# Kernel tuning notes

Measured on AMD Instinct MI355X. Metric: run time of the kernel, lower is better.

## Reference

```python
import jax, jax.numpy as jnp
import numpy as np
import math

N_HEADS = 16
N_POINTS = 4
EPS = 1e-6


def layer_norm(x, g, b):
    m = x.mean(-1, keepdims=True)
    v = ((x - m) ** 2).mean(-1, keepdims=True)
    return (x - m) / jnp.sqrt(v + EPS) * g + b


def ref_points(H, W, dtype):
    # matches CrossSelfAtt.get_reference_points for one square level -> (1, H*W, 1, 2) in (x, y)
    ys = (jnp.arange(H, dtype=dtype) + 0.5) / H
    xs = (jnp.arange(W, dtype=dtype) + 0.5) / W
    gy, gx = jnp.meshgrid(ys, xs, indexing='ij')
    return jnp.stack([gx.reshape(-1), gy.reshape(-1)], -1)[None, :, None, :]


def bilinear(v, H, W, loc):
    # v: (B, H*W, nH, Dh); loc: (B, Lq, nH, P, 2) normalized [0,1]; zero padding, align_corners=False
    B, _, nH, Dh = v.shape
    Lq, P = loc.shape[1], loc.shape[3]
    x = loc[..., 0] * W - 0.5
    y = loc[..., 1] * H - 0.5
    x0 = jnp.floor(x)
    y0 = jnp.floor(y)
    wx1 = x - x0
    wy1 = y - y0
    x0i = x0.astype(jnp.int32)
    y0i = y0.astype(jnp.int32)
    vt = v.transpose(0, 2, 1, 3)  # (B, nH, HW, Dh)

    def corner(xi, yi, w):
        valid = (xi >= 0) & (xi < W) & (yi >= 0) & (yi < H)
        idx = jnp.clip(yi, 0, H - 1) * W + jnp.clip(xi, 0, W - 1)  # (B, Lq, nH, P)
        idx_t = idx.transpose(0, 2, 1, 3).reshape(B, nH, Lq * P)
        g = jnp.take_along_axis(vt, idx_t[..., None], axis=2).reshape(B, nH, Lq, P, Dh)
        return g.transpose(0, 2, 1, 3, 4) * (w * valid)[..., None]

    return (corner(x0i, y0i, (1 - wx1) * (1 - wy1))
            + corner(x0i + 1, y0i, wx1 * (1 - wy1))
            + corner(x0i, y0i + 1, (1 - wx1) * wy1)
            + corner(x0i + 1, y0i + 1, wx1 * wy1))


def msda(query, value_in, shapes, ref, Wv, bv, Woff, boff, Wa, ba, Wo, bo):
    # standard Deformable-DETR MSDeformAttn forward
    B, Lq, D = query.shape
    nH, P, L = N_HEADS, N_POINTS, len(shapes)
    Dh = D // nH
    value = (value_in @ Wv + bv).reshape(B, -1, nH, Dh)
    off = (query @ Woff + boff).reshape(B, Lq, nH, L, P, 2)
    aw = jax.nn.softmax((query @ Wa + ba).reshape(B, Lq, nH, L * P), -1).reshape(B, Lq, nH, L, P)
    norm = jnp.asarray([[w_, h_] for (h_, w_) in shapes], dtype=query.dtype)  # (L, 2) = (W, H)
    loc = ref[:, :, None, :, None, :] + off / norm[None, None, None, :, None, :]
    out = jnp.zeros((B, Lq, nH, Dh), query.dtype)
    start = 0
    for l, (H_, W_) in enumerate(shapes):
        samp = bilinear(value[:, start:start + H_ * W_], H_, W_, loc[:, :, :, l])
        out = out + (samp * aw[:, :, :, l, :, None]).sum(3)
        start += H_ * W_
    return out.reshape(B, Lq, D) @ Wo + bo


def setup_inputs() -> dict:
    key = jax.random.key(0)
    B, Lq, Lf, D = 2, 4096, 4096, 768
    nH, P, L = N_HEADS, N_POINTS, 1
    ks = jax.random.split(key, 20)
    w = lambda k, s: jax.random.normal(k, s, jnp.float32) * 0.02
    return {
        'query': jax.random.normal(ks[0], (B, Lq, D), jnp.float32),
        'feat': jax.random.normal(ks[1], (B, Lf, D), jnp.float32),
        'spatial_shapes': jnp.array([[64, 64]], jnp.int32),
        'level_start_index': jnp.array([0], jnp.int32),
        'qn_W': w(ks[2], (D, D)), 'qn_b': jnp.zeros((D,)), 'qn_g': jnp.ones((D,)), 'qn_beta': jnp.zeros((D,)),
        'fn_W': w(ks[3], (D, D)), 'fn_b': jnp.zeros((D,)), 'fn_g': jnp.ones((D,)), 'fn_beta': jnp.zeros((D,)),
        'nm_g': jnp.ones((D,)), 'nm_beta': jnp.zeros((D,)),
        'gamma1': jax.random.normal(ks[4], (D,), jnp.float32) * 0.1,
        'c_Wv': w(ks[5], (D, D)), 'c_bv': jnp.zeros((D,)),
        'c_Woff': w(ks[6], (D, nH * L * P * 2)),
        'c_boff': jax.random.uniform(ks[7], (nH * L * P * 2,), jnp.float32, -3.0, 3.0),
        'c_Wa': w(ks[8], (D, nH * L * P)), 'c_ba': jnp.zeros((nH * L * P,)),
        'c_Wo': w(ks[9], (D, D)), 'c_bo': jnp.zeros((D,)),
        's_Wv': w(ks[10], (D, D)), 's_bv': jnp.zeros((D,)),
        's_Woff': w(ks[11], (D, nH * L * P * 2)),
        's_boff': jax.random.uniform(ks[12], (nH * L * P * 2,), jnp.float32, -3.0, 3.0),
        's_Wa': w(ks[13], (D, nH * L * P)), 's_ba': jnp.zeros((nH * L * P,)),
        's_Wo': w(ks[14], (D, D)), 's_bo': jnp.zeros((D,)),
    }


def reference(query, feat, spatial_shapes, level_start_index, qn_W, qn_b, qn_g, qn_beta, fn_W, fn_b, fn_g, fn_beta, nm_g, nm_beta, gamma1, c_Wv, c_bv, c_Woff, c_boff, c_Wa, c_ba, c_Wo, c_bo, s_Wv, s_bv, s_Woff, s_boff, s_Wa, s_ba, s_Wo, s_bo):
    shapes = [(int(h), int(w_)) for h, w_ in np.asarray(spatial_shapes)]
    qe = int(math.sqrt(query.shape[1]))
    ref = ref_points(qe, qe, query.dtype)  # (1, Lq, 1, 2)
    qn = layer_norm(query @ qn_W + qn_b, qn_g, qn_beta)
    fn = layer_norm(feat @ fn_W + fn_b, fn_g, fn_beta)
    attn = msda(qn, fn, shapes, ref, c_Wv, c_bv, c_Woff, c_boff, c_Wa, c_ba, c_Wo, c_bo)
    attn1 = layer_norm(attn, nm_g, nm_beta)
    attn2 = msda(attn1, attn1, [(qe, qe)], ref, s_Wv, s_bv, s_Woff, s_boff, s_Wa, s_ba, s_Wo, s_bo)
    # note: source uses gamma1 for BOTH terms (gamma2 is unused)
    return attn * gamma1 + attn2 * gamma1
```

## Files before the change

kernel.cpp:

```cpp
#include <hip/hip_runtime.h>
#include <hip/hip_bf16.h>
#include <math.h>

#define D_MODEL 768
#define NH 16
#define DH 48
#define NP 4
#define LQ 4096
#define BB 2
#define MTOT (BB * LQ)

typedef __attribute__((ext_vector_type(8))) _Float16 half8_t;
typedef __attribute__((ext_vector_type(4))) float floatx4;

__device__ __forceinline__ void load_lds16(const void* g, void* l) {
    __builtin_amdgcn_global_load_lds((const __attribute__((address_space(1))) void*)g,
                                     (__attribute__((address_space(3))) void*)l, 16, 0, 0);
}

template <int MODE>
__device__ __forceinline__ void gemm_body(
    const _Float16* __restrict__ A, const _Float16* __restrict__ Wt,
    const float* __restrict__ bias, float* __restrict__ C, int ldc,
    int tm, int tn,
    const float* __restrict__ attn, const float* __restrict__ gamma)
{
    constexpr int K = 768;
    constexpr int NT = K / 32;
    __shared__ _Float16 As[2][128 * 32];
    __shared__ _Float16 Bs[2][128 * 32];

    const int bm = tm * 128, bn = tn * 128;
    const int t = threadIdx.x;
    const int lane = t & 63;
    const int w = t >> 6;
    const int wm = (w >> 1) * 64, wn = (w & 1) * 64;

    floatx4 acc[4][4] = {};

    const int r0 = t >> 2;
    const int c8 = (t & 3) * 8;
    const size_t arow0 = (size_t)(bm + r0) * K + c8;
    const size_t arow1 = (size_t)(bm + 64 + r0) * K + c8;
    const size_t brow0 = (size_t)(bn + r0) * K + c8;
    const size_t brow1 = (size_t)(bn + 64 + r0) * K + c8;

    const int lrow = lane & 15;
    const int lk = (lane >> 4) * 8;

    load_lds16(A + arow0, &As[0][w * 512]);
    load_lds16(A + arow1, &As[0][2048 + w * 512]);
    load_lds16(Wt + brow0, &Bs[0][w * 512]);
    load_lds16(Wt + brow1, &Bs[0][2048 + w * 512]);
    __syncthreads();

    for (int ti = 0; ti < NT; ++ti) {
        const int cur = ti & 1;
        if (ti + 1 < NT) {
            const int kn = (ti + 1) * 32;
            const int nxt = cur ^ 1;
            load_lds16(A + arow0 + kn, &As[nxt][w * 512]);
            load_lds16(A + arow1 + kn, &As[nxt][2048 + w * 512]);
            load_lds16(Wt + brow0 + kn, &Bs[nxt][w * 512]);
            load_lds16(Wt + brow1 + kn, &Bs[nxt][2048 + w * 512]);
        }

        const _Float16* Ac = As[cur];
        const _Float16* Bc = Bs[cur];
        half8_t af[4], bf[4];
#pragma unroll
        for (int i = 0; i < 4; ++i) {
            af[i] = *(const half8_t*)&Ac[(wm + i * 16 + lrow) * 32 + lk];
            bf[i] = *(const half8_t*)&Bc[(wn + i * 16 + lrow) * 32 + lk];
        }
#pragma unroll
        for (int i = 0; i < 4; ++i)
#pragma unroll
            for (int j = 0; j < 4; ++j)
                acc[i][j] = __builtin_amdgcn_mfma_f32_16x16x32_f16(af[i], bf[j], acc[i][j], 0, 0, 0);

        if (ti + 1 < NT) __syncthreads();
    }

    const int rquad = (lane >> 4) * 4;
#pragma unroll
    for (int i = 0; i < 4; ++i) {
#pragma unroll
        for (int j = 0; j < 4; ++j) {
            const int col = bn + wn + j * 16 + lrow;
            const float bcol = bias[col];
#pragma unroll
            for (int r = 0; r < 4; ++r) {
                const size_t row = (size_t)(bm + wm + i * 16 + rquad + r);
                float v = acc[i][j][r] + bcol;
                if (MODE == 1) v = (attn[row * ldc + col] + v) * gamma[col];
                C[row * (size_t)ldc + col] = v;
            }
        }
    }
}

template <int MODE>
__global__ __launch_bounds__(256) void gemm_mfma(
    const _Float16* __restrict__ A, const _Float16* __restrict__ Wt,
    const float* __restrict__ bias, float* __restrict__ C,
    const float* __restrict__ attn, const float* __restrict__ gamma)
{
    const int bid = blockIdx.x;
    const int swz = (bid & 7) * 48 + (bid >> 3);
    gemm_body<MODE>(A, Wt, bias, C, 768, swz & 63, swz >> 6, attn, gamma);
}

__global__ __launch_bounds__(256) void dual_gemm(
    const _Float16* __restrict__ A0, const _Float16* __restrict__ W0,
    const float* __restrict__ b0, float* __restrict__ C0, int ldc0, int cnt0,
    const _Float16* __restrict__ A1, const _Float16* __restrict__ W1,
    const float* __restrict__ b1, float* __restrict__ C1, int ldc1, int cnt1)
{
    int bid = blockIdx.x;
    const _Float16 *A, *Wt; const float* bias; float* C; int ldc, cnt;
    if (bid < cnt0) { A = A0; Wt = W0; bias = b0; C = C0; ldc = ldc0; cnt = cnt0; }
    else { bid -= cnt0; A = A1; Wt = W1; bias = b1; C = C1; ldc = ldc1; cnt = cnt1; }
    const int q = cnt >> 3;
    const int swz = (bid & 7) * q + (bid >> 3);
    gemm_body<0>(A, Wt, bias, C, ldc, swz & 63, swz >> 6, nullptr, nullptr);
}

__device__ __forceinline__ void ln_wave_body(
    const float* __restrict__ X, _Float16* __restrict__ A,
    const float* __restrict__ g, const float* __restrict__ beta, int row)
{
    const int lane = threadIdx.x & 63;
    const float* x = X + (size_t)row * D_MODEL;
    float v[12];
    float s = 0.f, s2 = 0.f;
#pragma unroll
    for (int j = 0; j < 12; ++j) {
        v[j] = x[lane + 64 * j];
        s += v[j];
        s2 += v[j] * v[j];
    }
#pragma unroll
    for (int m = 1; m < 64; m <<= 1) {
        s += __shfl_xor(s, m);
        s2 += __shfl_xor(s2, m);
    }
    const float mean = s * (1.f / 768.f);
    const float var = s2 * (1.f / 768.f) - mean * mean;
    const float rstd = rsqrtf(var + 1e-6f);
    _Float16* arow = A + (size_t)row * D_MODEL;
#pragma unroll
    for (int j = 0; j < 12; ++j) {
        const int cc = lane + 64 * j;
        arow[cc] = (_Float16)((v[j] - mean) * rstd * g[cc] + beta[cc]);
    }
}

__global__ __launch_bounds__(256) void ln2_wave(
    const float* __restrict__ X0, _Float16* __restrict__ A0,
    const float* __restrict__ g0, const float* __restrict__ b0,
    const float* __restrict__ X1, _Float16* __restrict__ A1,
    const float* __restrict__ g1, const float* __restrict__ b1)
{
    const int r = blockIdx.x * 4 + (threadIdx.x >> 6);
    if (r < MTOT) ln_wave_body(X0, A0, g0, b0, r);
    else          ln_wave_body(X1, A1, g1, b1, r - MTOT);
}

__global__ __launch_bounds__(256) void ln_wave(
    const float* __restrict__ X, _Float16* __restrict__ A,
    const float* __restrict__ g, const float* __restrict__ beta)
{
    const int r = blockIdx.x * 4 + (threadIdx.x >> 6);
    ln_wave_body(X, A, g, beta, r);
}

__global__ __launch_bounds__(256) void convert_act2(
    const float* __restrict__ X0, _Float16* __restrict__ D0,
    const float* __restrict__ X1, _Float16* __restrict__ D1)
{
    const int i = blockIdx.x * 256 + threadIdx.x;
    const int sel = i / (MTOT * 192);
    const int r = i - sel * (MTOT * 192);
    const float* X = sel ? X1 : X0;
    _Float16* D = sel ? D1 : D0;
    const int c4 = r * 4;
    const float4 v = *(const float4*)(X + (size_t)c4);
    _Float16 o[4] = {(_Float16)v.x, (_Float16)v.y, (_Float16)v.z, (_Float16)v.w};
    *(uint2*)(D + (size_t)c4) = *(uint2*)o;
}

__global__ __launch_bounds__(256) void convert_w6(
    const float* __restrict__ w0, const float* __restrict__ w1,
    const float* __restrict__ w2, const float* __restrict__ w3,
    const float* __restrict__ w4, const float* __restrict__ w5,
    _Float16* __restrict__ Wall)
{
    const int wi = blockIdx.y;
    const float* W = (wi == 0) ? w0 : (wi == 1) ? w1 : (wi == 2) ? w2
                   : (wi == 3) ? w3 : (wi == 4) ? w4 : w5;
    _Float16* Wt = Wall + (size_t)wi * 768 * 768;

    __shared__ float tile[32][33];
    const int tk0 = (blockIdx.x / 24) * 32;
    const int tn0 = (blockIdx.x % 24) * 32;
    const int t = threadIdx.x;
#pragma unroll
    for (int r = 0; r < 4; ++r) {
        const int row = r * 8 + (t >> 5);
        const int col = t & 31;
        tile[row][col] = W[(size_t)(tk0 + row) * 768 + tn0 + col];
    }
    __syncthreads();
    const int n = t >> 3;
    const int kq = (t & 7) * 4;
    _Float16* dst = Wt + (size_t)(tn0 + n) * 768 + tk0 + kq;
#pragma unroll
    for (int u = 0; u < 4; ++u) dst[u] = (_Float16)tile[kq + u][n];
}

__global__ __launch_bounds__(256) void convert_offa(
    const float* __restrict__ Woff_c, const float* __restrict__ Wa_c,
    const float* __restrict__ boff_c, const float* __restrict__ ba_c,
    const float* __restrict__ Woff_s, const float* __restrict__ Wa_s,
    const float* __restrict__ boff_s, const float* __restrict__ ba_s,
    _Float16* __restrict__ Wc, _Float16* __restrict__ Ws,
    float* __restrict__ bias_c, float* __restrict__ bias_s)
{
    const int i = blockIdx.x * 256 + threadIdx.x;
    if (i >= 2 * 256 * 192) return;
    const int pair = i / (256 * 192);
    const int r = i - pair * (256 * 192);
    const int n = r / 192;
    const int k0 = (r - n * 192) * 4;
    const float* Woff = pair ? Woff_s : Woff_c;
    const float* Wa = pair ? Wa_s : Wa_c;
    _Float16* dst = pair ? Ws : Wc;
    _Float16* row = dst + (size_t)n * 768;
#pragma unroll
    for (int u = 0; u < 4; ++u) {
        const int k = k0 + u;
        float v = (n < 128) ? Woff[(size_t)k * 128 + n]
                : (n < 192) ? Wa[(size_t)k * 64 + (n - 128)] : 0.f;
        row[k] = (_Float16)v;
    }
    if (k0 == 0) {
        const float* boff = pair ? boff_s : boff_c;
        const float* ba = pair ? ba_s : ba_c;
        float* bias = pair ? bias_s : bias_c;
        bias[n] = (n < 128) ? boff[n] : (n < 192) ? ba[n - 128] : 0.f;
    }
}

__global__ __launch_bounds__(256) void offaw_post(
    const float* __restrict__ offc,
    float* __restrict__ loc, float* __restrict__ aw)
{
    const int i = blockIdx.x * 256 + threadIdx.x;
    if (i >= MTOT * NH) return;
    const int h = i & (NH - 1);
    const int bq = i >> 4;
    const int q = bq & (LQ - 1);

    const float* orow = offc + (size_t)bq * 256 + h * 8;
    const float* arow = offc + (size_t)bq * 256 + 128 + h * 4;

    float a0 = arow[0], a1 = arow[1], a2 = arow[2], a3 = arow[3];
    float mx = fmaxf(fmaxf(a0, a1), fmaxf(a2, a3));
    float e0 = expf(a0 - mx), e1 = expf(a1 - mx), e2 = expf(a2 - mx), e3 = expf(a3 - mx);
    float r = 1.f / (e0 + e1 + e2 + e3);

    const float refx = ((q & 63) + 0.5f) * (1.f / 64.f);
    const float refy = ((q >> 6) + 0.5f) * (1.f / 64.f);
#pragma unroll
    for (int p = 0; p < 4; ++p) {
        loc[(size_t)i * 8 + p * 2 + 0] = refx + orow[p * 2 + 0] * (1.f / 64.f);
        loc[(size_t)i * 8 + p * 2 + 1] = refy + orow[p * 2 + 1] * (1.f / 64.f);
    }
    aw[(size_t)i * 4 + 0] = e0 * r;
    aw[(size_t)i * 4 + 1] = e1 * r;
    aw[(size_t)i * 4 + 2] = e2 * r;
    aw[(size_t)i * 4 + 3] = e3 * r;
}

__global__ __launch_bounds__(256) void sample_f4(
    const float* __restrict__ value, const float* __restrict__ loc,
    const float* __restrict__ aw, _Float16* __restrict__ A)
{
    const int bid = blockIdx.x;
    const int swz = (bid & 7) * 768 + (bid >> 3);
    const int idx = swz * 256 + threadIdx.x;
    const int bqh = idx / 12;
    const int c = idx - bqh * 12;
    const int d0 = c * 4;
    const int h = bqh & (NH - 1);
    const int bq = bqh >> 4;
    const int b = bq >> 12;

    const float4 l01 = *(const float4*)(loc + (size_t)bqh * 8);
    const float4 l23 = *(const float4*)(loc + (size_t)bqh * 8 + 4);
    const float4 w4 = *(const float4*)(aw + (size_t)bqh * 4);
    const float lx[4] = {l01.x, l01.z, l23.x, l23.z};
    const float ly[4] = {l01.y, l01.w, l23.y, l23.w};
    const float wp4[4] = {w4.x, w4.y, w4.z, w4.w};

    const float* vbase = value + (size_t)b * LQ * D_MODEL + h * DH + d0;

    float4 acc = {0.f, 0.f, 0.f, 0.f};
#pragma unroll
    for (int p = 0; p < 4; ++p) {
        const float x = lx[p] * 64.f - 0.5f;
        const float y = ly[p] * 64.f - 0.5f;
        const float xf = floorf(x), yf = floorf(y);
        const float wx1 = x - xf, wy1 = y - yf;
        const float wx0 = 1.f - wx1, wy0 = 1.f - wy1;
        const int x0 = (int)xf, y0 = (int)yf;
        const int x1 = x0 + 1, y1 = y0 + 1;
        const float wp = wp4[p];
        const bool vx0 = (x0 >= 0) && (x0 < 64);
        const bool vx1 = (x1 >= 0) && (x1 < 64);
        const bool vy0 = (y0 >= 0) && (y0 < 64);
        const bool vy1 = (y1 >= 0) && (y1 < 64);
        const float cw[4] = {wp * wx0 * wy0, wp * wx1 * wy0, wp * wx0 * wy1, wp * wx1 * wy1};
        const bool cv[4] = {vx0 && vy0, vx1 && vy0, vx0 && vy1, vx1 && vy1};
        const int cxy[4][2] = {{x0, y0}, {x1, y0}, {x0, y1}, {x1, y1}};
#pragma unroll
        for (int k = 0; k < 4; ++k) {
            if (cv[k]) {
                const float4 g = *(const float4*)(vbase + (size_t)(cxy[k][1] * 64 + cxy[k][0]) * D_MODEL);
                acc.x += cw[k] * g.x; acc.y += cw[k] * g.y;
                acc.z += cw[k] * g.z; acc.w += cw[k] * g.w;
            }
        }
    }

    _Float16* arow = A + (size_t)bq * D_MODEL + h * DH + d0;
    _Float16 o[4] = {(_Float16)acc.x, (_Float16)acc.y, (_Float16)acc.z, (_Float16)acc.w};
    *(uint2*)arow = *(uint2*)o;
}

extern "C" void kernel_launch(void* const* d_in, const int* in_sizes, int n_in,
                              void* d_out, int out_size, void* d_ws, size_t ws_size,
                              hipStream_t stream)
{
    const float* query   = (const float*)d_in[0];
    const float* feat    = (const float*)d_in[1];
    const float* qn_W    = (const float*)d_in[4];
    const float* qn_b    = (const float*)d_in[5];
    const float* qn_g    = (const float*)d_in[6];
    const float* qn_beta = (const float*)d_in[7];
    const float* fn_W    = (const float*)d_in[8];
    const float* fn_b    = (const float*)d_in[9];
    const float* fn_g    = (const float*)d_in[10];
    const float* fn_beta = (const float*)d_in[11];
    const float* nm_g    = (const float*)d_in[12];
    const float* nm_beta = (const float*)d_in[13];
    const float* gamma1  = (const float*)d_in[14];
    const float* c_Wv    = (const float*)d_in[15];
    const float* c_bv    = (const float*)d_in[16];
    const float* c_Woff  = (const float*)d_in[17];
    const float* c_boff  = (const float*)d_in[18];
    const float* c_Wa    = (const float*)d_in[19];
    const float* c_ba    = (const float*)d_in[20];
    const float* c_Wo    = (const float*)d_in[21];
    const float* c_bo    = (const float*)d_in[22];
    const float* s_Wv    = (const float*)d_in[23];
    const float* s_bv    = (const float*)d_in[24];
    const float* s_Woff  = (const float*)d_in[25];
    const float* s_boff  = (const float*)d_in[26];
    const float* s_Wa    = (const float*)d_in[27];
    const float* s_ba    = (const float*)d_in[28];
    const float* s_Wo    = (const float*)d_in[29];
    const float* s_bo    = (const float*)d_in[30];

    float* ws = (float*)d_ws;
    const size_t SZ = (size_t)MTOT * D_MODEL;
    float* buf0 = ws;
    float* buf1 = ws + SZ;
    float* buf2 = ws + 2 * SZ;
    float* buf3 = ws + 3 * SZ;
    _Float16* slotA = (_Float16*)(ws + 4 * SZ);
    _Float16* slotB = (_Float16*)(ws + 4 * SZ + SZ / 2);
    float* loc    = ws + 5 * SZ;
    float* aws    = loc + (size_t)MTOT * 128;
    float* bias_c = aws + (size_t)MTOT * 64;
    float* bias_s = bias_c + 256;
    _Float16* W6 = (_Float16*)(bias_s + 256);
    _Float16* W_qn  = W6 + (size_t)0 * 768 * 768;
    _Float16* W_fn  = W6 + (size_t)1 * 768 * 768;
    _Float16* W_cWv = W6 + (size_t)2 * 768 * 768;
    _Float16* W_cWo = W6 + (size_t)3 * 768 * 768;
    _Float16* W_sWv = W6 + (size_t)4 * 768 * 768;
    _Float16* W_sWo = W6 + (size_t)5 * 768 * 768;
    _Float16* Woffa_c = W6 + (size_t)6 * 768 * 768;
    _Float16* Woffa_s = Woffa_c + (size_t)256 * 768;

    float* out = (float*)d_out;
    const dim3 blk(256);

    convert_w6<<<dim3(576, 6), blk, 0, stream>>>(qn_W, fn_W, c_Wv, c_Wo, s_Wv, s_Wo, W6);
    convert_offa<<<384, blk, 0, stream>>>(c_Woff, c_Wa, c_boff, c_ba,
                                          s_Woff, s_Wa, s_boff, s_ba,
                                          Woffa_c, Woffa_s, bias_c, bias_s);
    convert_act2<<<12288, blk, 0, stream>>>(query, slotA, feat, slotB);

    dual_gemm<<<768, blk, 0, stream>>>(slotA, W_qn, qn_b, buf0, 768, 384,
                                       slotB, W_fn, fn_b, buf1, 768, 384);
    ln2_wave<<<2 * MTOT / 4, blk, 0, stream>>>(buf0, slotA, qn_g, qn_beta,
                                               buf1, slotB, fn_g, fn_beta);
    dual_gemm<<<512, blk, 0, stream>>>(slotB, W_cWv, c_bv, buf2, 768, 384,
                                       slotA, Woffa_c, bias_c, buf0, 256, 128);
    offaw_post<<<(MTOT * NH + 255) / 256, blk, 0, stream>>>(buf0, loc, aws);
    sample_f4<<<MTOT * NH * 12 / 256, blk, 0, stream>>>(buf2, loc, aws, slotB);
    gemm_mfma<0><<<384, blk, 0, stream>>>(slotB, W_cWo, c_bo, buf3, nullptr, nullptr);

    ln_wave<<<MTOT / 4, blk, 0, stream>>>(buf3, slotA, nm_g, nm_beta);
    dual_gemm<<<512, blk, 0, stream>>>(slotA, W_sWv, s_bv, buf2, 768, 384,
                                       slotA, Woffa_s, bias_s, buf0, 256, 128);
    offaw_post<<<(MTOT * NH + 255) / 256, blk, 0, stream>>>(buf0, loc, aws);
    sample_f4<<<MTOT * NH * 12 / 256, blk, 0, stream>>>(buf2, loc, aws, slotB);
    gemm_mfma<1><<<384, blk, 0, stream>>>(slotB, W_sWo, s_bo, out, buf3, gamma1);
}
```

Measured before the change: 382.4 us.

## Store value projection in fp16, fuse offset post-processing into sampler, merge convert kernels

The value projection GEMM now writes fp16 output, and the bilinear sampler gathers half8 vectors instead of float4, which halves the gather traffic. The softmax and location computation from offaw_post moves into the sampler through shared memory, so the loc and aw round-trip through global memory and one launch per attention stage go away. The three conversion kernels become a single launch. The costs are fp16 rounding of the value tensor and 192-thread blocks in the sampler, where 32 threads do the preprocessing while the rest wait at a barrier.

```diff
diff --git a/kernel.cpp b/kernel.cpp
--- a/kernel.cpp
+++ b/kernel.cpp
@@ -21,7 +21,7 @@
 template <int MODE>
 __device__ __forceinline__ void gemm_body(
     const _Float16* __restrict__ A, const _Float16* __restrict__ Wt,
-    const float* __restrict__ bias, float* __restrict__ C, int ldc,
+    const float* __restrict__ bias, void* __restrict__ Cv, int ldc,
     int tm, int tn,
     const float* __restrict__ attn, const float* __restrict__ gamma)
 {
@@ -94,7 +94,8 @@
                 const size_t row = (size_t)(bm + wm + i * 16 + rquad + r);
                 float v = acc[i][j][r] + bcol;
                 if (MODE == 1) v = (attn[row * ldc + col] + v) * gamma[col];
-                C[row * (size_t)ldc + col] = v;
+                if (MODE == 2) ((_Float16*)Cv)[row * (size_t)ldc + col] = (_Float16)v;
+                else           ((float*)Cv)[row * (size_t)ldc + col] = v;
             }
         }
     }
@@ -103,7 +104,7 @@
 template <int MODE>
 __global__ __launch_bounds__(256) void gemm_mfma(
     const _Float16* __restrict__ A, const _Float16* __restrict__ Wt,
-    const float* __restrict__ bias, float* __restrict__ C,
+    const float* __restrict__ bias, void* __restrict__ C,
     const float* __restrict__ attn, const float* __restrict__ gamma)
 {
     const int bid = blockIdx.x;
@@ -111,19 +112,24 @@
     gemm_body<MODE>(A, Wt, bias, C, 768, swz & 63, swz >> 6, attn, gamma);
 }
 
+template <int M0, int M1>
 __global__ __launch_bounds__(256) void dual_gemm(
     const _Float16* __restrict__ A0, const _Float16* __restrict__ W0,
-    const float* __restrict__ b0, float* __restrict__ C0, int ldc0, int cnt0,
+    const float* __restrict__ b0, void* __restrict__ C0, int ldc0, int cnt0,
     const _Float16* __restrict__ A1, const _Float16* __restrict__ W1,
-    const float* __restrict__ b1, float* __restrict__ C1, int ldc1, int cnt1)
+    const float* __restrict__ b1, void* __restrict__ C1, int ldc1, int cnt1)
 {
     int bid = blockIdx.x;
-    const _Float16 *A, *Wt; const float* bias; float* C; int ldc, cnt;
-    if (bid < cnt0) { A = A0; Wt = W0; bias = b0; C = C0; ldc = ldc0; cnt = cnt0; }
-    else { bid -= cnt0; A = A1; Wt = W1; bias = b1; C = C1; ldc = ldc1; cnt = cnt1; }
-    const int q = cnt >> 3;
-    const int swz = (bid & 7) * q + (bid >> 3);
-    gemm_body<0>(A, Wt, bias, C, ldc, swz & 63, swz >> 6, nullptr, nullptr);
+    if (bid < cnt0) {
+        const int q = cnt0 >> 3;
+        const int swz = (bid & 7) * q + (bid >> 3);
+        gemm_body<M0>(A0, W0, b0, C0, ldc0, swz & 63, swz >> 6, nullptr, nullptr);
+    } else {
+        bid -= cnt0;
+        const int q = cnt1 >> 3;
+        const int swz = (bid & 7) * q + (bid >> 3);
+        gemm_body<M1>(A1, W1, b1, C1, ldc1, swz & 63, swz >> 6, nullptr, nullptr);
+    }
 }
 
 __device__ __forceinline__ void ln_wave_body(
@@ -175,51 +181,13 @@
     ln_wave_body(X, A, g, beta, r);
 }
 
-__global__ __launch_bounds__(256) void convert_act2(
-    const float* __restrict__ X0, _Float16* __restrict__ D0,
-    const float* __restrict__ X1, _Float16* __restrict__ D1)
-{
-    const int i = blockIdx.x * 256 + threadIdx.x;
-    const int sel = i / (MTOT * 192);
-    const int r = i - sel * (MTOT * 192);
-    const float* X = sel ? X1 : X0;
-    _Float16* D = sel ? D1 : D0;
-    const int c4 = r * 4;
-    const float4 v = *(const float4*)(X + (size_t)c4);
-    _Float16 o[4] = {(_Float16)v.x, (_Float16)v.y, (_Float16)v.z, (_Float16)v.w};
-    *(uint2*)(D + (size_t)c4) = *(uint2*)o;
-}
-
-__global__ __launch_bounds__(256) void convert_w6(
+__global__ __launch_bounds__(256) void convert_all(
+    const float* __restrict__ query, _Float16* __restrict__ actA,
+    const float* __restrict__ feat, _Float16* __restrict__ actB,
     const float* __restrict__ w0, const float* __restrict__ w1,
     const float* __restrict__ w2, const float* __restrict__ w3,
     const float* __restrict__ w4, const float* __restrict__ w5,
-    _Float16* __restrict__ Wall)
-{
-    const int wi = blockIdx.y;
-    const float* W = (wi == 0) ? w0 : (wi == 1) ? w1 : (wi == 2) ? w2
-                   : (wi == 3) ? w3 : (wi == 4) ? w4 : w5;
-    _Float16* Wt = Wall + (size_t)wi * 768 * 768;
-
-    __shared__ float tile[32][33];
-    const int tk0 = (blockIdx.x / 24) * 32;
-    const int tn0 = (blockIdx.x % 24) * 32;
-    const int t = threadIdx.x;
-#pragma unroll
-    for (int r = 0; r < 4; ++r) {
-        const int row = r * 8 + (t >> 5);
-        const int col = t & 31;
-        tile[row][col] = W[(size_t)(tk0 + row) * 768 + tn0 + col];
-    }
-    __syncthreads();
-    const int n = t >> 3;
-    const int kq = (t & 7) * 4;
-    _Float16* dst = Wt + (size_t)(tn0 + n) * 768 + tk0 + kq;
-#pragma unroll
-    for (int u = 0; u < 4; ++u) dst[u] = (_Float16)tile[kq + u][n];
-}
-
-__global__ __launch_bounds__(256) void convert_offa(
+    _Float16* __restrict__ Wall,
     const float* __restrict__ Woff_c, const float* __restrict__ Wa_c,
     const float* __restrict__ boff_c, const float* __restrict__ ba_c,
     const float* __restrict__ Woff_s, const float* __restrict__ Wa_s,
@@ -227,96 +195,122 @@
     _Float16* __restrict__ Wc, _Float16* __restrict__ Ws,
     float* __restrict__ bias_c, float* __restrict__ bias_s)
 {
-    const int i = blockIdx.x * 256 + threadIdx.x;
-    if (i >= 2 * 256 * 192) return;
-    const int pair = i / (256 * 192);
-    const int r = i - pair * (256 * 192);
-    const int n = r / 192;
-    const int k0 = (r - n * 192) * 4;
-    const float* Woff = pair ? Woff_s : Woff_c;
-    const float* Wa = pair ? Wa_s : Wa_c;
-    _Float16* dst = pair ? Ws : Wc;
-    _Float16* row = dst + (size_t)n * 768;
-#pragma unroll
-    for (int u = 0; u < 4; ++u) {
-        const int k = k0 + u;
-        float v = (n < 128) ? Woff[(size_t)k * 128 + n]
-                : (n < 192) ? Wa[(size_t)k * 64 + (n - 128)] : 0.f;
-        row[k] = (_Float16)v;
-    }
-    if (k0 == 0) {
-        const float* boff = pair ? boff_s : boff_c;
-        const float* ba = pair ? ba_s : ba_c;
-        float* bias = pair ? bias_s : bias_c;
-        bias[n] = (n < 128) ? boff[n] : (n < 192) ? ba[n - 128] : 0.f;
-    }
-}
-
-__global__ __launch_bounds__(256) void offaw_post(
-    const float* __restrict__ offc,
-    float* __restrict__ loc, float* __restrict__ aw)
-{
-    const int i = blockIdx.x * 256 + threadIdx.x;
-    if (i >= MTOT * NH) return;
-    const int h = i & (NH - 1);
-    const int bq = i >> 4;
-    const int q = bq & (LQ - 1);
-
-    const float* orow = offc + (size_t)bq * 256 + h * 8;
-    const float* arow = offc + (size_t)bq * 256 + 128 + h * 4;
-
-    float a0 = arow[0], a1 = arow[1], a2 = arow[2], a3 = arow[3];
-    float mx = fmaxf(fmaxf(a0, a1), fmaxf(a2, a3));
-    float e0 = expf(a0 - mx), e1 = expf(a1 - mx), e2 = expf(a2 - mx), e3 = expf(a3 - mx);
-    float r = 1.f / (e0 + e1 + e2 + e3);
-
-    const float refx = ((q & 63) + 0.5f) * (1.f / 64.f);
-    const float refy = ((q >> 6) + 0.5f) * (1.f / 64.f);
+    __shared__ float tile[32][33];
+    const int bid = blockIdx.x;
+    const int t = threadIdx.x;
+
+    if (bid < 12288) {
+        const int i = bid * 256 + t;
+        const int sel = i / (MTOT * 192);
+        const int r = i - sel * (MTOT * 192);
+        const float* X = sel ? feat : query;
+        _Float16* D = sel ? actB : actA;
+        const int c4 = r * 4;
+        const float4 v = *(const float4*)(X + (size_t)c4);
+        _Float16 o[4] = {(_Float16)v.x, (_Float16)v.y, (_Float16)v.z, (_Float16)v.w};
+        *(uint2*)(D + (size_t)c4) = *(uint2*)o;
+    } else if (bid < 15744) {
+        const int g = bid - 12288;
+        const int wi = g / 576;
+        const int gx = g - wi * 576;
+        const float* W = (wi == 0) ? w0 : (wi == 1) ? w1 : (wi == 2) ? w2
+                       : (wi == 3) ? w3 : (wi == 4) ? w4 : w5;
+        _Float16* Wt = Wall + (size_t)wi * 768 * 768;
+        const int tk0 = (gx / 24) * 32;
+        const int tn0 = (gx % 24) * 32;
+#pragma unroll
+        for (int r = 0; r < 4; ++r) {
+            const int row = r * 8 + (t >> 5);
+            const int col = t & 31;
+            tile[row][col] = W[(size_t)(tk0 + row) * 768 + tn0 + col];
+        }
+        __syncthreads();
+        const int n = t >> 3;
+        const int kq = (t & 7) * 4;
+        _Float16* dst = Wt + (size_t)(tn0 + n) * 768 + tk0 + kq;
+#pragma unroll
+        for (int u = 0; u < 4; ++u) dst[u] = (_Float16)tile[kq + u][n];
+    } else {
+        const int i = (bid - 15744) * 256 + t;
+        if (i >= 2 * 256 * 192) return;
+        const int pair = i / (256 * 192);
+        const int r = i - pair * (256 * 192);
+        const int n = r / 192;
+        const int k0 = (r - n * 192) * 4;
+        const float* Woff = pair ? Woff_s : Woff_c;
+        const float* Wa = pair ? Wa_s : Wa_c;
+        _Float16* dst = pair ? Ws : Wc;
+        _Float16* row = dst + (size_t)n * 768;
+#pragma unroll
+        for (int u = 0; u < 4; ++u) {
+            const int k = k0 + u;
+            float v = (n < 128) ? Woff[(size_t)k * 128 + n]
+                    : (n < 192) ? Wa[(size_t)k * 64 + (n - 128)] : 0.f;
+            row[k] = (_Float16)v;
+        }
+        if (k0 == 0) {
+            const float* boff = pair ? boff_s : boff_c;
+            const float* ba = pair ? ba_s : ba_c;
+            float* bias = pair ? bias_s : bias_c;
+            bias[n] = (n < 128) ? boff[n] : (n < 192) ? ba[n - 128] : 0.f;
+        }
+    }
+}
+
+__global__ __launch_bounds__(192) void sample_fused(
+    const _Float16* __restrict__ value, const float* __restrict__ offc,
+    _Float16* __restrict__ A)
+{
+    __shared__ float loc_s[32][8];
+    __shared__ float aw_s[32][4];
+
+    const int bid = blockIdx.x;
+    const int swz = (bid & 7) * 512 + (bid >> 3);
+    const int bq_base = swz * 2;
+    const int t = threadIdx.x;
+
+    if (t < 32) {
+        const int bq = bq_base + (t >> 4);
+        const int h = t & 15;
+        const int q = bq & (LQ - 1);
+        const float* orow = offc + (size_t)bq * 256 + h * 8;
+        const float* arow = offc + (size_t)bq * 256 + 128 + h * 4;
+        float a0 = arow[0], a1 = arow[1], a2 = arow[2], a3 = arow[3];
+        float mx = fmaxf(fmaxf(a0, a1), fmaxf(a2, a3));
+        float e0 = expf(a0 - mx), e1 = expf(a1 - mx), e2 = expf(a2 - mx), e3 = expf(a3 - mx);
+        float r = 1.f / (e0 + e1 + e2 + e3);
+        const float refx = ((q & 63) + 0.5f) * (1.f / 64.f);
+        const float refy = ((q >> 6) + 0.5f) * (1.f / 64.f);
+#pragma unroll
+        for (int p = 0; p < 4; ++p) {
+            loc_s[t][p * 2 + 0] = refx + orow[p * 2 + 0] * (1.f / 64.f);
+            loc_s[t][p * 2 + 1] = refy + orow[p * 2 + 1] * (1.f / 64.f);
+        }
+        aw_s[t][0] = e0 * r; aw_s[t][1] = e1 * r;
+        aw_s[t][2] = e2 * r; aw_s[t][3] = e3 * r;
+    }
+    __syncthreads();
+
+    const int lbqh = t / 6;
+    const int c = t - lbqh * 6;
+    const int d0 = c * 8;
+    const int bq = bq_base + (lbqh >> 4);
+    const int h = lbqh & 15;
+    const int b = bq >> 12;
+
+    const _Float16* vbase = value + (size_t)b * LQ * D_MODEL + h * DH + d0;
+
+    float acc[8] = {};
 #pragma unroll
     for (int p = 0; p < 4; ++p) {
-        loc[(size_t)i * 8 + p * 2 + 0] = refx + orow[p * 2 + 0] * (1.f / 64.f);
-        loc[(size_t)i * 8 + p * 2 + 1] = refy + orow[p * 2 + 1] * (1.f / 64.f);
-    }
-    aw[(size_t)i * 4 + 0] = e0 * r;
-    aw[(size_t)i * 4 + 1] = e1 * r;
-    aw[(size_t)i * 4 + 2] = e2 * r;
-    aw[(size_t)i * 4 + 3] = e3 * r;
-}
-
-__global__ __launch_bounds__(256) void sample_f4(
-    const float* __restrict__ value, const float* __restrict__ loc,
-    const float* __restrict__ aw, _Float16* __restrict__ A)
-{
-    const int bid = blockIdx.x;
-    const int swz = (bid & 7) * 768 + (bid >> 3);
-    const int idx = swz * 256 + threadIdx.x;
-    const int bqh = idx / 12;
-    const int c = idx - bqh * 12;
-    const int d0 = c * 4;
-    const int h = bqh & (NH - 1);
-    const int bq = bqh >> 4;
-    const int b = bq >> 12;
-
-    const float4 l01 = *(const float4*)(loc + (size_t)bqh * 8);
-    const float4 l23 = *(const float4*)(loc + (size_t)bqh * 8 + 4);
-    const float4 w4 = *(const float4*)(aw + (size_t)bqh * 4);
-    const float lx[4] = {l01.x, l01.z, l23.x, l23.z};
-    const float ly[4] = {l01.y, l01.w, l23.y, l23.w};
-    const float wp4[4] = {w4.x, w4.y, w4.z, w4.w};
-
-    const float* vbase = value + (size_t)b * LQ * D_MODEL + h * DH + d0;
-
-    float4 acc = {0.f, 0.f, 0.f, 0.f};
-#pragma unroll
-    for (int p = 0; p < 4; ++p) {
-        const float x = lx[p] * 64.f - 0.5f;
-        const float y = ly[p] * 64.f - 0.5f;
+        const float x = loc_s[lbqh][p * 2 + 0] * 64.f - 0.5f;
+        const float y = loc_s[lbqh][p * 2 + 1] * 64.f - 0.5f;
         const float xf = floorf(x), yf = floorf(y);
         const float wx1 = x - xf, wy1 = y - yf;
         const float wx0 = 1.f - wx1, wy0 = 1.f - wy1;
         const int x0 = (int)xf, y0 = (int)yf;
         const int x1 = x0 + 1, y1 = y0 + 1;
-        const float wp = wp4[p];
+        const float wp = aw_s[lbqh][p];
         const bool vx0 = (x0 >= 0) && (x0 < 64);
         const bool vx1 = (x1 >= 0) && (x1 < 64);
         const bool vy0 = (y0 >= 0) && (y0 < 64);
@@ -327,16 +321,18 @@
 #pragma unroll
         for (int k = 0; k < 4; ++k) {
             if (cv[k]) {
-                const float4 g = *(const float4*)(vbase + (size_t)(cxy[k][1] * 64 + cxy[k][0]) * D_MODEL);
-                acc.x += cw[k] * g.x; acc.y += cw[k] * g.y;
-                acc.z += cw[k] * g.z; acc.w += cw[k] * g.w;
+                const half8_t g = *(const half8_t*)(vbase + (size_t)(cxy[k][1] * 64 + cxy[k][0]) * D_MODEL);
+#pragma unroll
+                for (int u = 0; u < 8; ++u) acc[u] += cw[k] * (float)g[u];
             }
         }
     }
 
     _Float16* arow = A + (size_t)bq * D_MODEL + h * DH + d0;
-    _Float16 o[4] = {(_Float16)acc.x, (_Float16)acc.y, (_Float16)acc.z, (_Float16)acc.w};
-    *(uint2*)arow = *(uint2*)o;
+    _Float16 o[8];
+#pragma unroll
+    for (int u = 0; u < 8; ++u) o[u] = (_Float16)acc[u];
+    *(uint4*)arow = *(uint4*)o;
 }
 
 extern "C" void kernel_launch(void* const* d_in, const int* in_sizes, int n_in,
@@ -377,13 +373,11 @@
     const size_t SZ = (size_t)MTOT * D_MODEL;
     float* buf0 = ws;
     float* buf1 = ws + SZ;
-    float* buf2 = ws + 2 * SZ;
+    _Float16* val16 = (_Float16*)(ws + 2 * SZ);
     float* buf3 = ws + 3 * SZ;
     _Float16* slotA = (_Float16*)(ws + 4 * SZ);
     _Float16* slotB = (_Float16*)(ws + 4 * SZ + SZ / 2);
-    float* loc    = ws + 5 * SZ;
-    float* aws    = loc + (size_t)MTOT * 128;
-    float* bias_c = aws + (size_t)MTOT * 64;
+    float* bias_c = ws + 5 * SZ;
     float* bias_s = bias_c + 256;
     _Float16* W6 = (_Float16*)(bias_s + 256);
     _Float16* W_qn  = W6 + (size_t)0 * 768 * 768;
@@ -394,30 +388,29 @@
     _Float16* W_sWo = W6 + (size_t)5 * 768 * 768;
     _Float16* Woffa_c = W6 + (size_t)6 * 768 * 768;
     _Float16* Woffa_s = Woffa_c + (size_t)256 * 768;
+    float* offc = buf0;
 
     float* out = (float*)d_out;
     const dim3 blk(256);
 
-    convert_w6<<<dim3(576, 6), blk, 0, stream>>>(qn_W, fn_W, c_Wv, c_Wo, s_Wv, s_Wo, W6);
-    convert_offa<<<384, blk, 0, stream>>>(c_Woff, c_Wa, c_boff, c_ba,
-                                          s_Woff, s_Wa, s_boff, s_ba,
-                                          Woffa_c, Woffa_s, bias_c, bias_s);
-    convert_act2<<<12288, blk, 0, stream>>>(query, slotA, feat, slotB);
-
-    dual_gemm<<<768, blk, 0, stream>>>(slotA, W_qn, qn_b, buf0, 768, 384,
-                                       slotB, W_fn, fn_b, buf1, 768, 384);
+    convert_all<<<16128, blk, 0, stream>>>(
+        query, slotA, feat, slotB,
+        qn_W, fn_W, c_Wv, c_Wo, s_Wv, s_Wo, W6,
+        c_Woff, c_Wa, c_boff, c_ba, s_Woff, s_Wa, s_boff, s_ba,
+        Woffa_c, Woffa_s, bias_c, bias_s);
+
+    dual_gemm<0, 0><<<768, blk, 0, stream>>>(slotA, W_qn, qn_b, buf0, 768, 384,
+                                             slotB, W_fn, fn_b, buf1, 768, 384);
     ln2_wave<<<2 * MTOT / 4, blk, 0, stream>>>(buf0, slotA, qn_g, qn_beta,
                                                buf1, slotB, fn_g, fn_beta);
-    dual_gemm<<<512, blk, 0, stream>>>(slotB, W_cWv, c_bv, buf2, 768, 384,
-                                       slotA, Woffa_c, bias_c, buf0, 256, 128);
-    offaw_post<<<(MTOT * NH + 255) / 256, blk, 0, stream>>>(buf0, loc, aws);
-    sample_f4<<<MTOT * NH * 12 / 256, blk, 0, stream>>>(buf2, loc, aws, slotB);
+    dual_gemm<2, 0><<<512, blk, 0, stream>>>(slotB, W_cWv, c_bv, val16, 768, 384,
+                                             slotA, Woffa_c, bias_c, offc, 256, 128);
+    sample_fused<<<4096, dim3(192), 0, stream>>>(val16, offc, slotB);
     gemm_mfma<0><<<384, blk, 0, stream>>>(slotB, W_cWo, c_bo, buf3, nullptr, nullptr);
 
     ln_wave<<<MTOT / 4, blk, 0, stream>>>(buf3, slotA, nm_g, nm_beta);
-    dual_gemm<<<512, blk, 0, stream>>>(slotA, W_sWv, s_bv, buf2, 768, 384,
-                                       slotA, Woffa_s, bias_s, buf0, 256, 128);
-    offaw_post<<<(MTOT * NH + 255) / 256, blk, 0, stream>>>(buf0, loc, aws);
-    sample_f4<<<MTOT * NH * 12 / 256, blk, 0, stream>>>(buf2, loc, aws, slotB);
+    dual_gemm<2, 0><<<512, blk, 0, stream>>>(slotA, W_sWv, s_bv, val16, 768, 384,
+                                             slotA, Woffa_s, bias_s, offc, 256, 128);
+    sample_fused<<<4096, dim3(192), 0, stream>>>(val16, offc, slotB);
     gemm_mfma<1><<<384, blk, 0, stream>>>(slotB, W_sWo, s_bo, out, buf3, gamma1);
 }
```

After: 354.8 us. 7.2% less time.
